# Performance work log

Measured on AMD Instinct MI355X. Metric: run time of the kernel, lower is better.

Reference implementation:

```python
import jax, jax.numpy as jnp
import numpy as np

B, N, C, H, NL, NH = 8, 1024, 256, 512, 3, 8


def setup_inputs() -> dict:
    key = jax.random.key(0)
    ks = jax.random.split(key, 16)
    g = lambda k, shape: jax.random.normal(k, shape, jnp.float32) * 0.02
    return dict(
        concept_features=jax.random.normal(ks[0], (B, N, C), jnp.float32),
        adjacency_matrix=jax.random.uniform(ks[1], (B, N, N), jnp.float32),
        edge_types=jax.random.randint(ks[2], (B, N, N), 0, 10),
        concept_mask=jnp.ones((B, N), bool),
        W_emb=g(ks[3], (H, C)), b_emb=jnp.zeros((H,), jnp.float32),
        W_in=g(ks[4], (NL, 3 * H, H)), b_in=jnp.zeros((NL, 3 * H), jnp.float32),
        W_out=g(ks[5], (NL, H, H)), b_out=jnp.zeros((NL, H), jnp.float32),
        W_conv=g(ks[6], (NL, H, H)), b_conv=jnp.zeros((NL, H), jnp.float32),
        W_cls=g(ks[7], (1, H)), b_cls=jnp.zeros((1,), jnp.float32),
        W_diff=g(ks[8], (5, H)), b_diff=jnp.zeros((5,), jnp.float32),
        W_pre=g(ks[9], (1, 2 * H)), b_pre=jnp.zeros((1,), jnp.float32),
        W_pool=g(ks[10], (H, H)), b_pool=jnp.zeros((H,), jnp.float32),
    )


def reference(concept_features, adjacency_matrix, edge_types, concept_mask,
              W_emb, b_emb, W_in, b_in, W_out, b_out, W_conv, b_conv,
              W_cls, b_cls, W_diff, b_diff, W_pre, b_pre, W_pool, b_pool):
    Bq, Nc, _ = concept_features.shape
    Hd = W_emb.shape[0]
    dh = Hd // NH

    def mha(x, Wi, bi, Wo, bo):
        # torch nn.MultiheadAttention with batch_first=False: the (B,N,H)
        # input is treated as (seq=B, batch=N, embed=H) -> attention over B.
        qkv = x @ Wi.T + bi                      # (B,N,3H)
        q, k, v = jnp.split(qkv, 3, axis=-1)
        rs = lambda t: t.reshape(Bq, Nc, NH, dh)
        q, k, v = rs(q), rs(k), rs(v)
        sc = jnp.einsum('inhd,jnhd->nhij', q, k) / jnp.sqrt(jnp.float32(dh))
        a = jax.nn.softmax(sc, axis=-1)          # (N,NH,B,B)
        o = jnp.einsum('nhij,jnhd->inhd', a, v).reshape(Bq, Nc, Hd)
        return o @ Wo.T + bo

    def ln(x):  # F.layer_norm, no affine
        m = x.mean(-1, keepdims=True)
        v = ((x - m) ** 2).mean(-1, keepdims=True)
        return (x - m) * jax.lax.rsqrt(v + 1e-5)

    x = concept_features @ W_emb.T + b_emb       # (B,N,H)
    for l in range(W_in.shape[0]):
        att = mha(x, W_in[l], b_in[l], W_out[l], b_out[l])
        conv = att @ W_conv[l].T + b_conv[l]
        agg = jnp.einsum('bij,bjh->bih', adjacency_matrix, conv)
        x = ln(x + agg)

    mastery = x @ W_cls.T + b_cls                # (B,N,1)
    diff = x @ W_diff.T + b_diff                 # (B,N,5)

    # O(N^2) pairwise loop -> bilinear decomposition:
    # score(i,j) = x_i @ W_pre[:, :H].T + x_j @ W_pre[:, H:].T + b
    h1 = (x @ W_pre[:, :Hd].T)[..., 0]           # (B,N)
    h2 = (x @ W_pre[:, Hd:].T)[..., 0]           # (B,N)
    pair = h1[:, :, None] + h2[:, None, :] + b_pre[0]  # (B,N,N)
    off = ~np.eye(Nc, dtype=bool).reshape(-1)    # static mask, i!=j row-major
    prereq = pair.reshape(Bq, Nc * Nc)[:, off][..., None]  # (B,N*(N-1),1)

    graph = x.mean(axis=1) @ W_pool.T + b_pool   # (B,H)
    return (x, mastery, diff, prereq, graph)
```

## Files before the change

### kernel.cpp

```cpp
#include <hip/hip_runtime.h>
#include <hip/hip_bf16.h>

typedef unsigned short ushort_t;
typedef __attribute__((ext_vector_type(4))) float floatx4;
typedef __attribute__((ext_vector_type(8))) __bf16 bf16x8;
typedef __attribute__((ext_vector_type(4))) unsigned short ushortx4;
typedef __attribute__((ext_vector_type(8))) unsigned short ushortx8;

static __device__ __forceinline__ float b2f(ushort_t u) {
  union { unsigned int i; float f; } v; v.i = ((unsigned int)u) << 16; return v.f;
}
static __device__ __forceinline__ ushort_t f2b(float f) {
  unsigned int x = __float_as_uint(f);
  unsigned int r = (x + 0x7fffu + ((x >> 16) & 1u)) >> 16;
  return (ushort_t)r;
}
static __device__ __forceinline__ void glds16(const ushort_t* g, ushort_t* l) {
  __builtin_amdgcn_global_load_lds(
      (const __attribute__((address_space(1))) unsigned int*)g,
      (__attribute__((address_space(3))) unsigned int*)l, 16, 0, 0);
}

template<int MODE, bool ASPLIT, int KS>
__global__ __launch_bounds__(256, 3) void gemm_bt(
    const void* __restrict__ Ap, const ushort_t* __restrict__ Bm,
    const float* __restrict__ bias,
    ushort_t* __restrict__ C0, ushort_t* __restrict__ C1,
    ushort_t* __restrict__ C2, ushort_t* __restrict__ C3,
    int M, int N, int K, long aBatch, long bBatch, long cBatch)
{
  __shared__ __align__(16) ushort_t As[128 * 64];
  __shared__ __align__(16) ushort_t Bs[128 * 64];

  const int tid  = threadIdx.x;
  const int wid  = tid >> 6;
  const int lane = tid & 63;
  const int quad = lane >> 4;
  const int l16  = lane & 15;
  const int lin = blockIdx.y * gridDim.x + blockIdx.x;
  const int m0 = (lin % gridDim.y) * 128;
  const int n0 = (lin / gridDim.y) * 128;
  const int z  = (KS > 1) ? (int)(blockIdx.z / KS) : blockIdx.z;
  const int kq = (KS > 1) ? (int)(blockIdx.z % KS) : 0;
  const int kbeg = kq * (K / KS);
  const int kend = kbeg + (K / KS);
  ushort_t* outB = C0;
  if (KS >= 2 && kq == 1) outB = C1;
  if (KS >= 4 && kq == 2) outB = C2;
  if (KS >= 4 && kq == 3) outB = C3;

  const ushort_t* Ab = (const ushort_t*)Ap + (long)z * aBatch;
  const float*    Af = (const float*)Ap + (long)z * aBatch;
  Bm += (long)z * bBatch;

  const int wr = (wid >> 1) * 64;
  const int wc = (wid & 1) * 64;

  const int srow = tid >> 3;
  const int scj  = ((tid & 7) ^ (srow & 7)) * 8;
  const long abase = (long)(m0 + srow) * K + scj;
  const long bbase = (long)(n0 + srow) * K + scj;

  floatx4 acc[4][4];
#pragma unroll
  for (int i = 0; i < 4; ++i)
#pragma unroll
    for (int j = 0; j < 4; ++j) acc[i][j] = (floatx4){0.f, 0.f, 0.f, 0.f};

  const int rx = l16 & 7;

  for (int k0 = kbeg; k0 < kend; k0 += 64) {
    __syncthreads();
    if constexpr (ASPLIT) {
#pragma unroll
      for (int p = 0; p < 4; ++p)
        glds16(Ab + abase + 32 * p * (long)K + k0, &As[tid * 8 + p * 2048]);
    } else {
#pragma unroll
      for (int p = 0; p < 8; ++p) {
        int c = tid + p * 256;
        int row = c >> 4, sub4 = c & 15;
        floatx4 va = *(const floatx4*)(Af + (long)(m0 + row) * K + k0 + sub4 * 4);
        ushortx4 ah;
#pragma unroll
        for (int r = 0; r < 4; ++r) ah[r] = f2b(va[r]);
        int dst = row * 64 + (((sub4 >> 1) ^ (row & 7)) << 3) + ((sub4 & 1) << 2);
        *(ushortx4*)(&As[dst]) = ah;
      }
    }
#pragma unroll
    for (int p = 0; p < 4; ++p)
      glds16(Bm + bbase + 32 * p * (long)K + k0, &Bs[tid * 8 + p * 2048]);
    __syncthreads();

#pragma unroll
    for (int kk = 0; kk < 2; ++kk) {
      bf16x8 a[4], b[4];
#pragma unroll
      for (int i = 0; i < 4; ++i)
        a[i] = *(const bf16x8*)(&As[(wr + i * 16 + l16) * 64 +
                                    (((kk * 4 + quad) ^ rx) << 3)]);
#pragma unroll
      for (int j = 0; j < 4; ++j)
        b[j] = *(const bf16x8*)(&Bs[(wc + j * 16 + l16) * 64 +
                                    (((kk * 4 + quad) ^ rx) << 3)]);
#pragma unroll
      for (int i = 0; i < 4; ++i)
#pragma unroll
        for (int j = 0; j < 4; ++j)
          acc[i][j] = __builtin_amdgcn_mfma_f32_16x16x32_bf16(a[i], b[j], acc[i][j], 0, 0, 0);
    }
  }

#pragma unroll
  for (int j = 0; j < 4; ++j) {
    int col = n0 + wc + j * 16 + l16;
    float bv = (bias != nullptr) ? bias[col] : 0.f;
#pragma unroll
    for (int i = 0; i < 4; ++i) {
      int mbase = m0 + wr + i * 16 + quad * 4;
      if constexpr (MODE == 1) {
#pragma unroll
        for (int r = 0; r < 4; ++r)
          outB[(long)z * cBatch + (long)(mbase + r) * N + col] = f2b(acc[i][j][r] + bv);
      } else {
        int b = mbase >> 10, jrow = mbase & 1023;
        ushortx4 pk;
#pragma unroll
        for (int r = 0; r < 4; ++r) pk[r] = f2b(acc[i][j][r] + bv);
        *(ushortx4*)(outB + ((long)b * N + col) * 1024 + jrow) = pk;
      }
    }
  }
}

__global__ __launch_bounds__(256) void prep_kernel(
    const float* __restrict__ Win,  ushort_t* __restrict__ Winb,
    const float* __restrict__ Wemb, ushort_t* __restrict__ Wembb,
    const float* __restrict__ Wconv, ushort_t* __restrict__ Wcb,
    const float* __restrict__ ADJ,  ushort_t* __restrict__ ADJb,
    const float* __restrict__ Wout, ushort_t* __restrict__ WoT,
    const float* __restrict__ bout, const float* __restrict__ bconv,
    float* __restrict__ bfused,
    ushort_t* __restrict__ WembT,
    const float* __restrict__ bemb, const float* __restrict__ bin0,
    float* __restrict__ bfq)
{
  __shared__ float tile[64][65];
  const int bid = blockIdx.x, tid = threadIdx.x;
  if (bid < 5696) {
    const float* src; ushort_t* dst; long i;
    if (bid < 1152)      { src = Win;   dst = Winb;  i = (long)bid * 256 + tid; }
    else if (bid < 1216) { src = Wemb;  dst = Wembb; i = (long)(bid - 1152) * 256 + tid; }
    else if (bid < 1600) { src = Wconv; dst = Wcb;   i = (long)(bid - 1216) * 256 + tid; }
    else                 { src = ADJ;   dst = ADJb;  i = (long)(bid - 1600) * 256 + tid; }
    floatx4 a = ((const floatx4*)src)[2 * i];
    floatx4 b = ((const floatx4*)src)[2 * i + 1];
    ushortx4 ha, hb;
#pragma unroll
    for (int r = 0; r < 4; ++r) { ha[r] = f2b(a[r]); hb[r] = f2b(b[r]); }
    ((ushortx4*)dst)[2 * i] = ha; ((ushortx4*)dst)[2 * i + 1] = hb;
  } else if (bid < 5888) {
    const int t = bid - 5696;
    const int z = t >> 6, k0 = ((t >> 3) & 7) * 64, j0 = (t & 7) * 64;
    const long base = (long)z * 262144;
#pragma unroll
    for (int p = 0; p < 16; ++p) {
      int idx = tid + p * 256;
      int jj = idx >> 6, kk = idx & 63;
      tile[jj][kk] = Wout[base + (long)(j0 + jj) * 512 + k0 + kk];
    }
    __syncthreads();
#pragma unroll
    for (int p = 0; p < 16; ++p) {
      int idx = tid + p * 256;
      int kk = idx >> 6, jj = idx & 63;
      WoT[base + (long)(k0 + kk) * 512 + j0 + jj] = f2b(tile[jj][kk]);
    }
  } else if (bid < 5920) {
    const int t = bid - 5888;
    const int j0 = (t >> 2) * 64, k0 = (t & 3) * 64;
#pragma unroll
    for (int p = 0; p < 16; ++p) {
      int idx = tid + p * 256;
      int jj = idx >> 6, kk = idx & 63;
      tile[jj][kk] = Wemb[(long)(j0 + jj) * 256 + k0 + kk];
    }
    __syncthreads();
#pragma unroll
    for (int p = 0; p < 16; ++p) {
      int idx = tid + p * 256;
      int kk = idx >> 6, jj = idx & 63;
      WembT[(long)(k0 + kk) * 512 + j0 + jj] = f2b(tile[jj][kk]);
    }
  } else if (bid < 6304) {
    const int w = tid >> 6, lane = tid & 63;
    const int gi = (bid - 5920) * 4 + w;
    const int l = gi >> 9, o = gi & 511;
    float p = 0.f;
#pragma unroll
    for (int k = 0; k < 8; ++k)
      p += Wconv[(long)l * 262144 + (long)o * 512 + lane + 64 * k] *
           bout[l * 512 + lane + 64 * k];
#pragma unroll
    for (int msk = 1; msk <= 32; msk <<= 1) p += __shfl_xor(p, msk);
    if (lane == 0) bfused[gi] = p + bconv[l * 512 + o];
  } else {
    const int w = tid >> 6, lane = tid & 63;
    const int o = (bid - 6304) * 4 + w;
    float p = 0.f;
#pragma unroll
    for (int k = 0; k < 8; ++k)
      p += Win[(long)o * 512 + lane + 64 * k] * bemb[lane + 64 * k];
#pragma unroll
    for (int msk = 1; msk <= 32; msk <<= 1) p += __shfl_xor(p, msk);
    if (lane == 0) bfq[o] = p + bin0[o];
  }
}

__global__ __launch_bounds__(512) void attn_kernel(
    const ushort_t* __restrict__ qkv, ushort_t* __restrict__ outp)
{
  __shared__ float qs[8 * 1540];
  __shared__ float aw[8][64];
  const int tid = threadIdx.x;
  const int n = blockIdx.x;

  const ushort_t* src = qkv + (long)n * 1536;
#pragma unroll
  for (int p = 0; p < 3; ++p) {
    int c = tid + p * 512;
    int i = c / 192, off = (c % 192) * 8;
    ushortx8 u = *(const ushortx8*)(src + (long)i * 1024 * 1536 + off);
    float* d = &qs[i * 1540 + off];
#pragma unroll
    for (int r = 0; r < 8; ++r) d[r] = b2f(u[r]);
  }
  __syncthreads();

  const int h    = tid >> 6;
  const int lane = tid & 63;
  const int i = lane >> 3, j = lane & 7;
  float s = 0.f;
#pragma unroll 8
  for (int d = 0; d < 64; ++d)
    s += qs[i * 1540 + h * 64 + d] * qs[j * 1540 + 512 + h * 64 + d];
  s *= 0.125f;

  float m = s;
  m = fmaxf(m, __shfl_xor(m, 1));
  m = fmaxf(m, __shfl_xor(m, 2));
  m = fmaxf(m, __shfl_xor(m, 4));
  float e = __expf(s - m);
  float sum = e;
  sum += __shfl_xor(sum, 1);
  sum += __shfl_xor(sum, 2);
  sum += __shfl_xor(sum, 4);
  aw[h][lane] = e / sum;

  const long ob = (long)n * 512 + h * 64 + lane;
#pragma unroll
  for (int ii = 0; ii < 8; ++ii) {
    float acc = 0.f;
#pragma unroll
    for (int jj = 0; jj < 8; ++jj)
      acc += aw[h][ii * 8 + jj] * qs[jj * 1540 + 1024 + h * 64 + lane];
    outp[ob + (long)ii * 1024 * 512] = f2b(acc);
  }
}

__global__ __launch_bounds__(256) void ln_kernel(
    const ushort_t* __restrict__ xb,
    const ushort_t* __restrict__ aggA, const ushort_t* __restrict__ aggB,
    ushort_t* __restrict__ outB)
{
  const int w = threadIdx.x >> 6, lane = threadIdx.x & 63;
  const long base = ((long)blockIdx.x * 4 + w) * 512;
  float v[8];
  float s = 0.f;
#pragma unroll
  for (int k = 0; k < 8; ++k) {
    long idx = base + lane + 64 * k;
    v[k] = b2f(xb[idx]) + b2f(aggA[idx]) + b2f(aggB[idx]);
    s += v[k];
  }
#pragma unroll
  for (int msk = 1; msk <= 32; msk <<= 1) s += __shfl_xor(s, msk);
  float mean = s * (1.f / 512.f);
  float vv = 0.f;
#pragma unroll
  for (int k = 0; k < 8; ++k) { float d = v[k] - mean; vv += d * d; }
#pragma unroll
  for (int msk = 1; msk <= 32; msk <<= 1) vv += __shfl_xor(vv, msk);
  float inv = rsqrtf(vv * (1.f / 512.f) + 1e-5f);
#pragma unroll
  for (int k = 0; k < 8; ++k)
    outB[base + lane + 64 * k] = f2b((v[k] - mean) * inv);
}

__global__ __launch_bounds__(256) void final_ln_heads_kernel(
    const ushort_t* __restrict__ xb,
    const ushort_t* __restrict__ aggA, const ushort_t* __restrict__ aggB,
    float* __restrict__ out_x,
    const float* __restrict__ Wcls, const float* __restrict__ bcls,
    const float* __restrict__ Wdiff, const float* __restrict__ bdiff,
    const float* __restrict__ Wpre,
    float* __restrict__ mastery, float* __restrict__ diff,
    float* __restrict__ h1, float* __restrict__ h2,
    float* __restrict__ xp)
{
  __shared__ float sp4[4][512];
  const int w = threadIdx.x >> 6, lane = threadIdx.x & 63;
  const long row = (long)blockIdx.x * 4 + w;
  const long base = row * 512;
  float v[8];
  float s = 0.f;
#pragma unroll
  for (int k = 0; k < 8; ++k) {
    long idx = base + lane + 64 * k;
    v[k] = b2f(xb[idx]) + b2f(aggA[idx]) + b2f(aggB[idx]);
    s += v[k];
  }
#pragma unroll
  for (int msk = 1; msk <= 32; msk <<= 1) s += __shfl_xor(s, msk);
  float mean = s * (1.f / 512.f);
  float vv = 0.f;
#pragma unroll
  for (int k = 0; k < 8; ++k) { float d = v[k] - mean; vv += d * d; }
#pragma unroll
  for (int msk = 1; msk <= 32; msk <<= 1) vv += __shfl_xor(vv, msk);
  float inv = rsqrtf(vv * (1.f / 512.f) + 1e-5f);
#pragma unroll
  for (int k = 0; k < 8; ++k) {
    v[k] = (v[k] - mean) * inv;
    out_x[base + lane + 64 * k] = v[k];
    sp4[w][lane + 64 * k] = v[k];
  }
  __syncthreads();
  for (int t = threadIdx.x; t < 512; t += 256)
    xp[(long)blockIdx.x * 512 + t] =
        sp4[0][t] + sp4[1][t] + sp4[2][t] + sp4[3][t];
#pragma unroll
  for (int o = 0; o < 8; ++o) {
    const float* wp = (o == 0) ? Wcls
                    : (o <= 5) ? (Wdiff + (o - 1) * 512)
                    : (o == 6) ? Wpre : (Wpre + 512);
    float p = 0.f;
#pragma unroll
    for (int k = 0; k < 8; ++k) p += v[k] * wp[lane + 64 * k];
#pragma unroll
    for (int msk = 1; msk <= 32; msk <<= 1) p += __shfl_xor(p, msk);
    if (lane == 0) {
      if (o == 0)      mastery[row] = p + bcls[0];
      else if (o <= 5) diff[row * 5 + (o - 1)] = p + bdiff[o - 1];
      else if (o == 6) h1[row] = p;
      else             h2[row] = p;
    }
  }
}

__global__ __launch_bounds__(256) void epi_kernel(
    const float* __restrict__ h1, const float* __restrict__ h2,
    const float* __restrict__ bpre, float* __restrict__ outp,
    const float* __restrict__ xp, float* __restrict__ xm)
{
  const int bid = blockIdx.x;
  if (bid < 8192) {
    const int b = bid >> 10, i = bid & 1023;
    const float base = h1[b * 1024 + i] + bpre[0];
    const long ob = (long)b * (1024 * 1023) + (long)i * 1023;
#pragma unroll
    for (int r = 0; r < 4; ++r) {
      int j = r * 256 + threadIdx.x;
      if (j == i) continue;
      int pos = (j < i) ? j : j - 1;
      outp[ob + pos] = base + h2[b * 1024 + j];
    }
  } else {
    const int gi = (bid - 8192) * 256 + threadIdx.x;
    const int b = gi >> 9, c = gi & 511;
    const float* p = xp + (long)b * 256 * 512 + c;
    float s = 0.f;
    for (int q = 0; q < 256; ++q) s += p[q * 512];
    xm[b * 512 + c] = s;
  }
}

__global__ __launch_bounds__(256) void graph_kernel(
    const float* __restrict__ xm, const float* __restrict__ Wpool,
    const float* __restrict__ bpool, float* __restrict__ g)
{
  const int gi = blockIdx.x * 256 + threadIdx.x;
  const int b = gi >> 9, o = gi & 511;
  float s = 0.f;
  for (int hh = 0; hh < 512; ++hh) s += xm[b * 512 + hh] * Wpool[o * 512 + hh];
  g[gi] = s * (1.f / 1024.f) + bpool[o];
}

extern "C" void kernel_launch(void* const* d_in, const int* in_sizes, int n_in,
                              void* d_out, int out_size, void* d_ws, size_t ws_size,
                              hipStream_t stream)
{
  const float* CF    = (const float*)d_in[0];
  const float* ADJ   = (const float*)d_in[1];
  const float* Wemb  = (const float*)d_in[4];
  const float* bemb  = (const float*)d_in[5];
  const float* Win   = (const float*)d_in[6];
  const float* bin   = (const float*)d_in[7];
  const float* Wout  = (const float*)d_in[8];
  const float* bout  = (const float*)d_in[9];
  const float* Wconv = (const float*)d_in[10];
  const float* bconv = (const float*)d_in[11];
  const float* Wcls  = (const float*)d_in[12];
  const float* bcls  = (const float*)d_in[13];
  const float* Wdiff = (const float*)d_in[14];
  const float* bdiff = (const float*)d_in[15];
  const float* Wpre  = (const float*)d_in[16];
  const float* bpre  = (const float*)d_in[17];
  const float* Wpool = (const float*)d_in[18];
  const float* bpool = (const float*)d_in[19];

  ushort_t* W = (ushort_t*)d_ws;
  ushort_t* xb   = W;
  ushort_t* qkvb = W + 4194304;
  ushort_t* cT    = qkvb;
  ushort_t* aggA  = qkvb + 4194304;
  ushort_t* aggB  = qkvb + 8388608;
  ushort_t* WoT   = qkvb + 4194304;
  ushort_t* Wembb = qkvb + 4980736;
  ushort_t* Wcb   = qkvb + 5111808;
  ushort_t* WembT = qkvb + 5898240;
  ushort_t* Winb = W + 16777216;
  ushort_t* Wfb  = W + 19136512;
  ushort_t* ADJb = W + 19922944;
  ushort_t* Wie  = W + 28311552;
  float* bfused = (float*)(W + 28704768);
  float* bfq    = bfused + 1536;
  float* h1     = bfq + 1536;
  float* h2     = h1 + 8192;
  float* xm     = h2 + 8192;
  float* xp     = xm + 4096;

  float* out_x       = (float*)d_out;
  float* out_mastery = out_x + 4194304;
  float* out_diff    = out_mastery + 8192;
  float* out_prereq  = out_diff + 40960;
  float* out_graph   = out_prereq + 8380416;
  ushort_t* aob = (ushort_t*)out_x;

  dim3 blk(256);

  prep_kernel<<<dim3(6688), blk, 0, stream>>>(
      Win, Winb, Wemb, Wembb, Wconv, Wcb, ADJ, ADJb,
      Wout, WoT, bout, bconv, bfused, WembT, bemb, bin, bfq);
  gemm_bt<1, true, 1><<<dim3(2, 12, 1), blk, 0, stream>>>(
      Winb, WembT, nullptr, Wie, nullptr, nullptr, nullptr,
      1536, 256, 512, 0, 0, 0);
  gemm_bt<1, true, 1><<<dim3(4, 4, 3), blk, 0, stream>>>(
      Wcb, WoT, nullptr, Wfb, nullptr, nullptr, nullptr,
      512, 512, 512, 262144, 262144, 262144);

  gemm_bt<1, false, 1><<<dim3(4, 64, 1), blk, 0, stream>>>(
      CF, Wembb, bemb, xb, nullptr, nullptr, nullptr, 8192, 512, 256, 0, 0, 0);

  for (int l = 0; l < 3; ++l) {
    if (l == 0) {
      gemm_bt<1, false, 1><<<dim3(12, 64, 1), blk, 0, stream>>>(
          CF, Wie, bfq, qkvb, nullptr, nullptr, nullptr,
          8192, 1536, 256, 0, 0, 0);
    } else {
      gemm_bt<1, true, 1><<<dim3(12, 64, 1), blk, 0, stream>>>(
          xb, Winb + (long)l * 786432, bin + l * 1536,
          qkvb, nullptr, nullptr, nullptr, 8192, 1536, 512, 0, 0, 0);
    }
    attn_kernel<<<dim3(1024), dim3(512), 0, stream>>>(qkvb, aob);
    gemm_bt<2, true, 1><<<dim3(4, 64, 1), blk, 0, stream>>>(
        aob, Wfb + (long)l * 262144, bfused + l * 512,
        cT, nullptr, nullptr, nullptr, 8192, 512, 512, 0, 0, 0);
    gemm_bt<1, true, 2><<<dim3(4, 8, 16), blk, 0, stream>>>(
        ADJb, cT, nullptr, aggA, aggB, nullptr, nullptr,
        1024, 512, 1024, 1048576, 524288, 524288);
    if (l < 2)
      ln_kernel<<<dim3(2048), blk, 0, stream>>>(xb, aggA, aggB, xb);
    else
      final_ln_heads_kernel<<<dim3(2048), blk, 0, stream>>>(
          xb, aggA, aggB, out_x, Wcls, bcls, Wdiff, bdiff, Wpre,
          out_mastery, out_diff, h1, h2, xp);
  }

  epi_kernel<<<dim3(8208), blk, 0, stream>>>(h1, h2, bpre, out_prereq,
                                             xp, xm);
  graph_kernel<<<dim3(16), blk, 0, stream>>>(xm, Wpool, bpool, out_graph);
}
```

Before: 459.1 us.

## Fuse embedding into layer-0 QKV GEMM, split adjacency K four ways, trim attention

Concept features are converted to bf16 in the prep kernel, which removes the fp32 A-load path from the GEMM. The embedding and layer-0 QKV projections become one GEMM with a concatenated weight and bias, and a new output mode scatters columns into x and qkv. The adjacency GEMM now splits K four ways instead of two, with the extra partials stored in the prereq output buffer and summed in the layer-norm kernels. The attention kernel keeps q/k/v in bf16 shared memory with vectorised dot products and caches V in registers. Risks include the extra partial-sum traffic and reusing the output buffer as scratch before the epilogue overwrites it.

```diff
diff --git a/kernel.cpp b/kernel.cpp
--- a/kernel.cpp
+++ b/kernel.cpp
@@ -21,9 +21,9 @@
       (__attribute__((address_space(3))) unsigned int*)l, 16, 0, 0);
 }
 
-template<int MODE, bool ASPLIT, int KS>
+template<int MODE, int KS>
 __global__ __launch_bounds__(256, 3) void gemm_bt(
-    const void* __restrict__ Ap, const ushort_t* __restrict__ Bm,
+    const ushort_t* __restrict__ Ab, const ushort_t* __restrict__ Bm,
     const float* __restrict__ bias,
     ushort_t* __restrict__ C0, ushort_t* __restrict__ C1,
     ushort_t* __restrict__ C2, ushort_t* __restrict__ C3,
@@ -49,8 +49,7 @@
   if (KS >= 4 && kq == 2) outB = C2;
   if (KS >= 4 && kq == 3) outB = C3;
 
-  const ushort_t* Ab = (const ushort_t*)Ap + (long)z * aBatch;
-  const float*    Af = (const float*)Ap + (long)z * aBatch;
+  Ab += (long)z * aBatch;
   Bm += (long)z * bBatch;
 
   const int wr = (wid >> 1) * 64;
@@ -71,23 +70,9 @@
 
   for (int k0 = kbeg; k0 < kend; k0 += 64) {
     __syncthreads();
-    if constexpr (ASPLIT) {
-#pragma unroll
-      for (int p = 0; p < 4; ++p)
-        glds16(Ab + abase + 32 * p * (long)K + k0, &As[tid * 8 + p * 2048]);
-    } else {
-#pragma unroll
-      for (int p = 0; p < 8; ++p) {
-        int c = tid + p * 256;
-        int row = c >> 4, sub4 = c & 15;
-        floatx4 va = *(const floatx4*)(Af + (long)(m0 + row) * K + k0 + sub4 * 4);
-        ushortx4 ah;
-#pragma unroll
-        for (int r = 0; r < 4; ++r) ah[r] = f2b(va[r]);
-        int dst = row * 64 + (((sub4 >> 1) ^ (row & 7)) << 3) + ((sub4 & 1) << 2);
-        *(ushortx4*)(&As[dst]) = ah;
-      }
-    }
+#pragma unroll
+    for (int p = 0; p < 4; ++p)
+      glds16(Ab + abase + 32 * p * (long)K + k0, &As[tid * 8 + p * 2048]);
 #pragma unroll
     for (int p = 0; p < 4; ++p)
       glds16(Bm + bbase + 32 * p * (long)K + k0, &Bs[tid * 8 + p * 2048]);
@@ -123,12 +108,19 @@
 #pragma unroll
         for (int r = 0; r < 4; ++r)
           outB[(long)z * cBatch + (long)(mbase + r) * N + col] = f2b(acc[i][j][r] + bv);
-      } else {
+      } else if constexpr (MODE == 2) {
         int b = mbase >> 10, jrow = mbase & 1023;
         ushortx4 pk;
 #pragma unroll
         for (int r = 0; r < 4; ++r) pk[r] = f2b(acc[i][j][r] + bv);
         *(ushortx4*)(outB + ((long)b * N + col) * 1024 + jrow) = pk;
+      } else {
+        ushort_t* o = (n0 < 512) ? C0 : C1;
+        const int cw = (n0 < 512) ? 512 : 1536;
+        const int cc = (n0 < 512) ? col : col - 512;
+#pragma unroll
+        for (int r = 0; r < 4; ++r)
+          o[(long)(mbase + r) * cw + cc] = f2b(acc[i][j][r] + bv);
       }
     }
   }
@@ -136,32 +128,34 @@
 
 __global__ __launch_bounds__(256) void prep_kernel(
     const float* __restrict__ Win,  ushort_t* __restrict__ Winb,
-    const float* __restrict__ Wemb, ushort_t* __restrict__ Wembb,
+    const float* __restrict__ Wemb, ushort_t* __restrict__ Wq0,
     const float* __restrict__ Wconv, ushort_t* __restrict__ Wcb,
     const float* __restrict__ ADJ,  ushort_t* __restrict__ ADJb,
+    const float* __restrict__ CF,   ushort_t* __restrict__ CFb,
     const float* __restrict__ Wout, ushort_t* __restrict__ WoT,
     const float* __restrict__ bout, const float* __restrict__ bconv,
     float* __restrict__ bfused,
     ushort_t* __restrict__ WembT,
     const float* __restrict__ bemb, const float* __restrict__ bin0,
-    float* __restrict__ bfq)
+    float* __restrict__ bcat)
 {
   __shared__ float tile[64][65];
   const int bid = blockIdx.x, tid = threadIdx.x;
-  if (bid < 5696) {
+  if (bid < 6720) {
     const float* src; ushort_t* dst; long i;
-    if (bid < 1152)      { src = Win;   dst = Winb;  i = (long)bid * 256 + tid; }
-    else if (bid < 1216) { src = Wemb;  dst = Wembb; i = (long)(bid - 1152) * 256 + tid; }
-    else if (bid < 1600) { src = Wconv; dst = Wcb;   i = (long)(bid - 1216) * 256 + tid; }
-    else                 { src = ADJ;   dst = ADJb;  i = (long)(bid - 1600) * 256 + tid; }
+    if (bid < 1152)      { src = Win;   dst = Winb; i = (long)bid * 256 + tid; }
+    else if (bid < 1216) { src = Wemb;  dst = Wq0;  i = (long)(bid - 1152) * 256 + tid; }
+    else if (bid < 1600) { src = Wconv; dst = Wcb;  i = (long)(bid - 1216) * 256 + tid; }
+    else if (bid < 5696) { src = ADJ;   dst = ADJb; i = (long)(bid - 1600) * 256 + tid; }
+    else                 { src = CF;    dst = CFb;  i = (long)(bid - 5696) * 256 + tid; }
     floatx4 a = ((const floatx4*)src)[2 * i];
     floatx4 b = ((const floatx4*)src)[2 * i + 1];
     ushortx4 ha, hb;
 #pragma unroll
     for (int r = 0; r < 4; ++r) { ha[r] = f2b(a[r]); hb[r] = f2b(b[r]); }
     ((ushortx4*)dst)[2 * i] = ha; ((ushortx4*)dst)[2 * i + 1] = hb;
-  } else if (bid < 5888) {
-    const int t = bid - 5696;
+  } else if (bid < 6912) {
+    const int t = bid - 6720;
     const int z = t >> 6, k0 = ((t >> 3) & 7) * 64, j0 = (t & 7) * 64;
     const long base = (long)z * 262144;
 #pragma unroll
@@ -177,8 +171,8 @@
       int kk = idx >> 6, jj = idx & 63;
       WoT[base + (long)(k0 + kk) * 512 + j0 + jj] = f2b(tile[jj][kk]);
     }
-  } else if (bid < 5920) {
-    const int t = bid - 5888;
+  } else if (bid < 6944) {
+    const int t = bid - 6912;
     const int j0 = (t >> 2) * 64, k0 = (t & 3) * 64;
 #pragma unroll
     for (int p = 0; p < 16; ++p) {
@@ -193,9 +187,9 @@
       int kk = idx >> 6, jj = idx & 63;
       WembT[(long)(k0 + kk) * 512 + j0 + jj] = f2b(tile[jj][kk]);
     }
-  } else if (bid < 6304) {
+  } else if (bid < 7328) {
     const int w = tid >> 6, lane = tid & 63;
-    const int gi = (bid - 5920) * 4 + w;
+    const int gi = (bid - 6944) * 4 + w;
     const int l = gi >> 9, o = gi & 511;
     float p = 0.f;
 #pragma unroll
@@ -205,23 +199,26 @@
 #pragma unroll
     for (int msk = 1; msk <= 32; msk <<= 1) p += __shfl_xor(p, msk);
     if (lane == 0) bfused[gi] = p + bconv[l * 512 + o];
-  } else {
+  } else if (bid < 7712) {
     const int w = tid >> 6, lane = tid & 63;
-    const int o = (bid - 6304) * 4 + w;
+    const int o = (bid - 7328) * 4 + w;
     float p = 0.f;
 #pragma unroll
     for (int k = 0; k < 8; ++k)
       p += Win[(long)o * 512 + lane + 64 * k] * bemb[lane + 64 * k];
 #pragma unroll
     for (int msk = 1; msk <= 32; msk <<= 1) p += __shfl_xor(p, msk);
-    if (lane == 0) bfq[o] = p + bin0[o];
-  }
-}
-
-__global__ __launch_bounds__(512) void attn_kernel(
+    if (lane == 0) bcat[512 + o] = p + bin0[o];
+  } else {
+    int idx = (bid - 7712) * 256 + tid;
+    bcat[idx] = bemb[idx];
+  }
+}
+
+__global__ __launch_bounds__(512, 8) void attn_kernel(
     const ushort_t* __restrict__ qkv, ushort_t* __restrict__ outp)
 {
-  __shared__ float qs[8 * 1540];
+  __shared__ ushort_t qs[8 * 1544];
   __shared__ float aw[8][64];
   const int tid = threadIdx.x;
   const int n = blockIdx.x;
@@ -231,20 +228,24 @@
   for (int p = 0; p < 3; ++p) {
     int c = tid + p * 512;
     int i = c / 192, off = (c % 192) * 8;
-    ushortx8 u = *(const ushortx8*)(src + (long)i * 1024 * 1536 + off);
-    float* d = &qs[i * 1540 + off];
-#pragma unroll
-    for (int r = 0; r < 8; ++r) d[r] = b2f(u[r]);
+    *(ushortx8*)(&qs[i * 1544 + off]) =
+        *(const ushortx8*)(src + (long)i * 1024 * 1536 + off);
   }
   __syncthreads();
 
   const int h    = tid >> 6;
   const int lane = tid & 63;
   const int i = lane >> 3, j = lane & 7;
+  const ushort_t* qrow = &qs[i * 1544 + h * 64];
+  const ushort_t* krow = &qs[j * 1544 + 512 + h * 64];
   float s = 0.f;
-#pragma unroll 8
-  for (int d = 0; d < 64; ++d)
-    s += qs[i * 1540 + h * 64 + d] * qs[j * 1540 + 512 + h * 64 + d];
+#pragma unroll
+  for (int c8 = 0; c8 < 8; ++c8) {
+    ushortx8 qa = *(const ushortx8*)(qrow + c8 * 8);
+    ushortx8 ka = *(const ushortx8*)(krow + c8 * 8);
+#pragma unroll
+    for (int r = 0; r < 8; ++r) s += b2f(qa[r]) * b2f(ka[r]);
+  }
   s *= 0.125f;
 
   float m = s;
@@ -258,13 +259,16 @@
   sum += __shfl_xor(sum, 4);
   aw[h][lane] = e / sum;
 
+  float vv[8];
+#pragma unroll
+  for (int jj = 0; jj < 8; ++jj)
+    vv[jj] = b2f(qs[jj * 1544 + 1024 + h * 64 + lane]);
   const long ob = (long)n * 512 + h * 64 + lane;
 #pragma unroll
   for (int ii = 0; ii < 8; ++ii) {
     float acc = 0.f;
 #pragma unroll
-    for (int jj = 0; jj < 8; ++jj)
-      acc += aw[h][ii * 8 + jj] * qs[jj * 1540 + 1024 + h * 64 + lane];
+    for (int jj = 0; jj < 8; ++jj) acc += aw[h][ii * 8 + jj] * vv[jj];
     outp[ob + (long)ii * 1024 * 512] = f2b(acc);
   }
 }
@@ -272,6 +276,7 @@
 __global__ __launch_bounds__(256) void ln_kernel(
     const ushort_t* __restrict__ xb,
     const ushort_t* __restrict__ aggA, const ushort_t* __restrict__ aggB,
+    const ushort_t* __restrict__ aggC, const ushort_t* __restrict__ aggD,
     ushort_t* __restrict__ outB)
 {
   const int w = threadIdx.x >> 6, lane = threadIdx.x & 63;
@@ -281,7 +286,8 @@
 #pragma unroll
   for (int k = 0; k < 8; ++k) {
     long idx = base + lane + 64 * k;
-    v[k] = b2f(xb[idx]) + b2f(aggA[idx]) + b2f(aggB[idx]);
+    v[k] = b2f(xb[idx]) + b2f(aggA[idx]) + b2f(aggB[idx]) +
+           b2f(aggC[idx]) + b2f(aggD[idx]);
     s += v[k];
   }
 #pragma unroll
@@ -301,6 +307,7 @@
 __global__ __launch_bounds__(256) void final_ln_heads_kernel(
     const ushort_t* __restrict__ xb,
     const ushort_t* __restrict__ aggA, const ushort_t* __restrict__ aggB,
+    const ushort_t* __restrict__ aggC, const ushort_t* __restrict__ aggD,
     float* __restrict__ out_x,
     const float* __restrict__ Wcls, const float* __restrict__ bcls,
     const float* __restrict__ Wdiff, const float* __restrict__ bdiff,
@@ -318,7 +325,8 @@
 #pragma unroll
   for (int k = 0; k < 8; ++k) {
     long idx = base + lane + 64 * k;
-    v[k] = b2f(xb[idx]) + b2f(aggA[idx]) + b2f(aggB[idx]);
+    v[k] = b2f(xb[idx]) + b2f(aggA[idx]) + b2f(aggB[idx]) +
+           b2f(aggC[idx]) + b2f(aggD[idx]);
     s += v[k];
   }
 #pragma unroll
@@ -427,16 +435,16 @@
   ushort_t* aggA  = qkvb + 4194304;
   ushort_t* aggB  = qkvb + 8388608;
   ushort_t* WoT   = qkvb + 4194304;
-  ushort_t* Wembb = qkvb + 4980736;
-  ushort_t* Wcb   = qkvb + 5111808;
-  ushort_t* WembT = qkvb + 5898240;
+  ushort_t* Wcb   = qkvb + 4980736;
+  ushort_t* WembT = qkvb + 5767168;
   ushort_t* Winb = W + 16777216;
   ushort_t* Wfb  = W + 19136512;
   ushort_t* ADJb = W + 19922944;
-  ushort_t* Wie  = W + 28311552;
-  float* bfused = (float*)(W + 28704768);
-  float* bfq    = bfused + 1536;
-  float* h1     = bfq + 1536;
+  ushort_t* CFb  = W + 28311552;
+  ushort_t* Wq0  = W + 32505856;
+  float* bfused = (float*)(W + 33030144);
+  float* bcat   = bfused + 1536;
+  float* h1     = bcat + 2048;
   float* h2     = h1 + 8192;
   float* xm     = h2 + 8192;
   float* xp     = xm + 4096;
@@ -447,44 +455,43 @@
   float* out_prereq  = out_diff + 40960;
   float* out_graph   = out_prereq + 8380416;
   ushort_t* aob = (ushort_t*)out_x;
+  ushort_t* aggC = (ushort_t*)out_prereq;
+  ushort_t* aggD = (ushort_t*)out_prereq + 4194304;
 
   dim3 blk(256);
 
-  prep_kernel<<<dim3(6688), blk, 0, stream>>>(
-      Win, Winb, Wemb, Wembb, Wconv, Wcb, ADJ, ADJb,
-      Wout, WoT, bout, bconv, bfused, WembT, bemb, bin, bfq);
-  gemm_bt<1, true, 1><<<dim3(2, 12, 1), blk, 0, stream>>>(
-      Winb, WembT, nullptr, Wie, nullptr, nullptr, nullptr,
+  prep_kernel<<<dim3(7714), blk, 0, stream>>>(
+      Win, Winb, Wemb, Wq0, Wconv, Wcb, ADJ, ADJb, CF, CFb,
+      Wout, WoT, bout, bconv, bfused, WembT, bemb, bin, bcat);
+  gemm_bt<1, 1><<<dim3(2, 12, 1), blk, 0, stream>>>(
+      Winb, WembT, nullptr, Wq0 + 512 * 256, nullptr, nullptr, nullptr,
       1536, 256, 512, 0, 0, 0);
-  gemm_bt<1, true, 1><<<dim3(4, 4, 3), blk, 0, stream>>>(
+  gemm_bt<1, 1><<<dim3(4, 4, 3), blk, 0, stream>>>(
       Wcb, WoT, nullptr, Wfb, nullptr, nullptr, nullptr,
       512, 512, 512, 262144, 262144, 262144);
 
-  gemm_bt<1, false, 1><<<dim3(4, 64, 1), blk, 0, stream>>>(
-      CF, Wembb, bemb, xb, nullptr, nullptr, nullptr, 8192, 512, 256, 0, 0, 0);
-
   for (int l = 0; l < 3; ++l) {
     if (l == 0) {
-      gemm_bt<1, false, 1><<<dim3(12, 64, 1), blk, 0, stream>>>(
-          CF, Wie, bfq, qkvb, nullptr, nullptr, nullptr,
-          8192, 1536, 256, 0, 0, 0);
+      gemm_bt<3, 1><<<dim3(16, 64, 1), blk, 0, stream>>>(
+          CFb, Wq0, bcat, xb, qkvb, nullptr, nullptr,
+          8192, 2048, 256, 0, 0, 0);
     } else {
-      gemm_bt<1, true, 1><<<dim3(12, 64, 1), blk, 0, stream>>>(
+      gemm_bt<1, 1><<<dim3(12, 64, 1), blk, 0, stream>>>(
           xb, Winb + (long)l * 786432, bin + l * 1536,
           qkvb, nullptr, nullptr, nullptr, 8192, 1536, 512, 0, 0, 0);
     }
     attn_kernel<<<dim3(1024), dim3(512), 0, stream>>>(qkvb, aob);
-    gemm_bt<2, true, 1><<<dim3(4, 64, 1), blk, 0, stream>>>(
+    gemm_bt<2, 1><<<dim3(4, 64, 1), blk, 0, stream>>>(
         aob, Wfb + (long)l * 262144, bfused + l * 512,
         cT, nullptr, nullptr, nullptr, 8192, 512, 512, 0, 0, 0);
-    gemm_bt<1, true, 2><<<dim3(4, 8, 16), blk, 0, stream>>>(
-        ADJb, cT, nullptr, aggA, aggB, nullptr, nullptr,
+    gemm_bt<1, 4><<<dim3(4, 8, 32), blk, 0, stream>>>(
+        ADJb, cT, nullptr, aggA, aggB, aggC, aggD,
         1024, 512, 1024, 1048576, 524288, 524288);
     if (l < 2)
-      ln_kernel<<<dim3(2048), blk, 0, stream>>>(xb, aggA, aggB, xb);
+      ln_kernel<<<dim3(2048), blk, 0, stream>>>(xb, aggA, aggB, aggC, aggD, xb);
     else
       final_ln_heads_kernel<<<dim3(2048), blk, 0, stream>>>(
-          xb, aggA, aggB, out_x, Wcls, bcls, Wdiff, bdiff, Wpre,
+          xb, aggA, aggB, aggC, aggD, out_x, Wcls, bcls, Wdiff, bdiff, Wpre,
           out_mastery, out_diff, h1, h2, xp);
   }
 
```

Measured after the change: 451.0 us. About the same (-1.8%).
